# Kernel optimization log

Measured on AMD Instinct MI355X. Metric: run time of the kernel, lower is better.

Reference implementation:

```python
import jax, jax.numpy as jnp
import numpy as np

EMB = 1024

def setup_inputs() -> dict:
    key = jax.random.key(0)
    ks = jax.random.split(key, 6)
    T, k1, k2, D = 64, 256, 1024, EMB
    scale = 1.0 / np.sqrt(D)
    return {
        "fast_feature": jax.random.normal(ks[0], (T, k2, D), jnp.float32),
        "slow_feature": jax.random.normal(ks[1], (T, k1, D), jnp.float32),
        "fast_W": jax.random.normal(ks[2], (D, D), jnp.float32) * scale,
        "fast_b": jax.random.normal(ks[3], (D,), jnp.float32) * 0.01,
        "slow_W": jax.random.normal(ks[4], (D, D), jnp.float32) * scale,
        "slow_b": jax.random.normal(ks[5], (D,), jnp.float32) * 0.01,
    }

def reference(fast_feature, slow_feature, fast_W, fast_b, slow_W, slow_b):
    # Linear projections (torch Linear: x @ W.T + b)
    fast_key = jnp.einsum('tkd,ed->tke', fast_feature, fast_W) + fast_b  # [T,k2,D]
    slow_key = jnp.einsum('tkd,ed->tke', slow_feature, slow_W) + slow_b  # [T,k1,D]
    # Scaled dot-product similarity fast->slow
    sim = jnp.einsum('tqd,tkd->tqk', fast_key, slow_key)  # [T,k2,k1]
    sim = sim / jnp.sqrt(jnp.asarray(slow_feature.shape[-1], sim.dtype))
    attn = jax.nn.softmax(sim, axis=-1)
    ctx = jnp.einsum('tqk,tkd->tqd', attn, slow_feature)  # note: values are raw slow_feature
    return fast_feature + ctx
```

## Files before the change

### kernel.cpp

```cpp
#include <hip/hip_runtime.h>
#include <stdint.h>

typedef __attribute__((ext_vector_type(8))) short bf16x8;
typedef __attribute__((ext_vector_type(4))) float f32x4;

#define BM 128
#define BN 128
#define BK 64

__device__ __forceinline__ unsigned short f2bf(float f) {
  unsigned int u = __builtin_bit_cast(unsigned int, f);
  u += 0x7FFFu + ((u >> 16) & 1u);
  return (unsigned short)(u >> 16);
}

__device__ __forceinline__ void gload_lds16(const void* g, void* l) {
  __builtin_amdgcn_global_load_lds(
      (__attribute__((address_space(1))) void*)(uintptr_t)g,
      (__attribute__((address_space(3))) void*)l,
      16, 0, 0);
}

template <int MODE>
__global__ __launch_bounds__(256, 2) void gemm_bt(
    const unsigned short* __restrict__ A, const unsigned short* __restrict__ B,
    void* __restrict__ Cv, const float* __restrict__ aux, int M, int N, int K,
    int nm, int nn, int nb, long sAB, long sBB, long sCB, long sXB, float scale)
{
  __shared__ __align__(16) unsigned short sAt[BM * BK];
  __shared__ __align__(16) unsigned short sBt[BN * BK];

  const int tid = threadIdx.x;
  const int lane = tid & 63;
  const int wid = tid >> 6;

  int nwg = nm * nn * nb;
  int id = blockIdx.x;
  int swz = (id & 7) * (nwg >> 3) + (id >> 3);
  int t = swz / (nm * nn);
  int rem = swz - t * (nm * nn);
  int mi = rem / nn;
  int ni = rem - mi * nn;

  const long bm = (long)mi * BM;
  const long bn = (long)ni * BN;

  const unsigned short* Ag = A + (long)t * sAB + bm * K;
  const unsigned short* Bg = B + (long)t * sBB + bn * K;

  f32x4 acc[4][4];
#pragma unroll
  for (int i = 0; i < 4; i++)
#pragma unroll
    for (int j = 0; j < 4; j++)
#pragma unroll
      for (int r = 0; r < 4; r++) acc[i][j][r] = 0.f;

  const int wm = (wid >> 1) * 64;
  const int wn = (wid & 1) * 64;
  const int fr = lane & 15;
  const int fq = lane >> 4;

  const int lrow = wid * 32 + (lane >> 3);
  const int lcolb = (lane & 7) * 16;

  for (int k0 = 0; k0 < K; k0 += BK) {
#pragma unroll
    for (int c = 0; c < 4; ++c) {
      int r = lrow + c * 8;
      gload_lds16((const char*)(Ag + (long)r * K + k0) + lcolb,
                  (char*)sAt + wid * 4096 + c * 1024);
      gload_lds16((const char*)(Bg + (long)r * K + k0) + lcolb,
                  (char*)sBt + wid * 4096 + c * 1024);
    }
    __syncthreads();
#pragma unroll
    for (int kk = 0; kk < BK; kk += 32) {
      bf16x8 af[4], bb[4];
#pragma unroll
      for (int i = 0; i < 4; i++)
        af[i] = *(const bf16x8*)&sAt[(wm + i * 16 + fr) * BK + kk + fq * 8];
#pragma unroll
      for (int j = 0; j < 4; j++)
        bb[j] = *(const bf16x8*)&sBt[(wn + j * 16 + fr) * BK + kk + fq * 8];
#pragma unroll
      for (int i = 0; i < 4; i++)
#pragma unroll
        for (int j = 0; j < 4; j++)
          acc[i][j] = __builtin_amdgcn_mfma_f32_16x16x32_bf16(af[i], bb[j], acc[i][j], 0, 0, 0);
    }
    __syncthreads();
  }

#pragma unroll
  for (int i = 0; i < 4; i++) {
    long grow0 = bm + wm + i * 16 + fq * 4;
#pragma unroll
    for (int j = 0; j < 4; j++) {
      long gcol = bn + wn + j * 16 + fr;
      if (MODE == 0) {
        unsigned short* C = (unsigned short*)Cv + (long)t * sCB;
        float b = aux[gcol];
#pragma unroll
        for (int r = 0; r < 4; r++)
          C[(grow0 + r) * N + gcol] = f2bf(acc[i][j][r] + b);
      } else if (MODE == 1) {
        float* C = (float*)Cv + (long)t * sCB;
#pragma unroll
        for (int r = 0; r < 4; r++)
          C[(grow0 + r) * N + gcol] = acc[i][j][r] * scale;
      } else {
        float* C = (float*)Cv + (long)t * sCB;
        const float* X = aux + (long)t * sXB;
#pragma unroll
        for (int r = 0; r < 4; r++) {
          long idx = (grow0 + r) * N + gcol;
          C[idx] = acc[i][j][r] + X[idx];
        }
      }
    }
  }
}

__global__ __launch_bounds__(256) void convert_f32_bf16(
    const float* __restrict__ in, unsigned short* __restrict__ out, long n) {
  long i = ((long)blockIdx.x * 256 + threadIdx.x) * 4;
  long stride = (long)gridDim.x * 1024;
  for (; i < n; i += stride) {
    float4 v = *(const float4*)(in + i);
    ushort4 o;
    o.x = f2bf(v.x); o.y = f2bf(v.y); o.z = f2bf(v.z); o.w = f2bf(v.w);
    *(ushort4*)(out + i) = o;
  }
}

__global__ __launch_bounds__(256) void transpose_slow_bf16(
    const float* __restrict__ in, unsigned short* __restrict__ out) {
  __shared__ unsigned short tile[32][33];
  int t = blockIdx.z;
  int d0 = blockIdx.x * 32;
  int k0 = blockIdx.y * 32;
  const float* ip = in + (long)t * 256 * 1024;
  unsigned short* op = out + (long)t * 1024 * 256;
  int tx = threadIdx.x & 31, ty = threadIdx.x >> 5;
#pragma unroll
  for (int p = 0; p < 4; p++) {
    int k = ty + p * 8;
    tile[k][tx] = f2bf(ip[(long)(k0 + k) * 1024 + d0 + tx]);
  }
  __syncthreads();
#pragma unroll
  for (int p = 0; p < 4; p++) {
    int d = ty + p * 8;
    op[(long)(d0 + d) * 256 + k0 + tx] = tile[tx][d];
  }
}

__global__ __launch_bounds__(256) void softmax256(
    const float* __restrict__ sim, unsigned short* __restrict__ attn) {
  int row = blockIdx.x * 4 + (threadIdx.x >> 6);
  int lane = threadIdx.x & 63;
  const float4 v = *(const float4*)(sim + (long)row * 256 + lane * 4);
  float m = fmaxf(fmaxf(v.x, v.y), fmaxf(v.z, v.w));
#pragma unroll
  for (int o = 32; o >= 1; o >>= 1) m = fmaxf(m, __shfl_xor(m, o));
  float e0 = __expf(v.x - m), e1 = __expf(v.y - m);
  float e2 = __expf(v.z - m), e3 = __expf(v.w - m);
  float s = e0 + e1 + e2 + e3;
#pragma unroll
  for (int o = 32; o >= 1; o >>= 1) s += __shfl_xor(s, o);
  float inv = 1.0f / s;
  ushort4 o4;
  o4.x = f2bf(e0 * inv); o4.y = f2bf(e1 * inv);
  o4.z = f2bf(e2 * inv); o4.w = f2bf(e3 * inv);
  *(ushort4*)(attn + (long)row * 256 + lane * 4) = o4;
}

extern "C" void kernel_launch(void* const* d_in, const int* in_sizes, int n_in,
                              void* d_out, int out_size, void* d_ws, size_t ws_size,
                              hipStream_t stream) {
  const float* fastF     = (const float*)d_in[0];
  const float* slowF     = (const float*)d_in[1];
  const float* fastW     = (const float*)d_in[2];
  const float* fast_bias = (const float*)d_in[3];
  const float* slowW     = (const float*)d_in[4];
  const float* slow_bias = (const float*)d_in[5];
  float* out = (float*)d_out;

  char* ws = (char*)d_ws;
  unsigned short* fastBf  = (unsigned short*)(ws);
  float*          sim     = (float*)(ws);
  unsigned short* attnBf  = (unsigned short*)(ws + 67108864L);
  unsigned short* fastKey = (unsigned short*)(ws + 134217728L);
  unsigned short* slowBf  = (unsigned short*)(ws + 268435456L);
  unsigned short* slowT   = (unsigned short*)(ws + 301989888L);
  unsigned short* slowKey = (unsigned short*)(ws + 335544320L);
  unsigned short* fWb     = (unsigned short*)(ws + 369098752L);
  unsigned short* sWb     = (unsigned short*)(ws + 371195904L);

  convert_f32_bf16<<<2048, 256, 0, stream>>>(fastF, fastBf, 67108864L);
  convert_f32_bf16<<<2048, 256, 0, stream>>>(slowF, slowBf, 16777216L);
  convert_f32_bf16<<<1024, 256, 0, stream>>>(fastW, fWb, 1048576L);
  convert_f32_bf16<<<1024, 256, 0, stream>>>(slowW, sWb, 1048576L);
  transpose_slow_bf16<<<dim3(32, 8, 64), 256, 0, stream>>>(slowF, slowT);

  gemm_bt<0><<<128 * 8, 256, 0, stream>>>(slowBf, sWb, slowKey, slow_bias,
      16384, 1024, 1024, 128, 8, 1, 0, 0, 0, 0, 1.f);
  gemm_bt<0><<<512 * 8, 256, 0, stream>>>(fastBf, fWb, fastKey, fast_bias,
      65536, 1024, 1024, 512, 8, 1, 0, 0, 0, 0, 1.f);
  gemm_bt<1><<<8 * 2 * 64, 256, 0, stream>>>(fastKey, slowKey, sim, nullptr,
      1024, 256, 1024, 8, 2, 64, 1048576L, 262144L, 262144L, 0, 0.03125f);
  softmax256<<<16384, 256, 0, stream>>>(sim, attnBf);
  gemm_bt<2><<<8 * 8 * 64, 256, 0, stream>>>(attnBf, slowT, out, fastF,
      1024, 1024, 256, 8, 8, 64, 262144L, 262144L, 1048576L, 1048576L, 1.f);
}
```

Baseline: 576.6 us.

## Replace GEMM with 256x256 8-wave double-buffered pipelined kernel

Rewrites the batched bf16 GEMM to use 256x256 tiles with 512 threads (8 waves), a 128 KB double-buffered LDS region with XOR-swizzled layout, and staged async global->LDS loads interleaved with MFMA quadrants under explicit vmcnt waits and barriers. Goals are to raise arithmetic intensity per tile, hide global load latency behind compute, and avoid LDS bank conflicts. The cost is larger LDS use, which limits occupancy, and fewer workgroups for the smaller GEMMs (e.g. the sim GEMM has 256 blocks), which may underfill the GPU.

Measured after the change: 497.4 us. 13.7% less time.

```diff
diff --git a/kernel.cpp b/kernel.cpp
--- a/kernel.cpp
+++ b/kernel.cpp
@@ -3,10 +3,6 @@
 
 typedef __attribute__((ext_vector_type(8))) short bf16x8;
 typedef __attribute__((ext_vector_type(4))) float f32x4;
-
-#define BM 128
-#define BN 128
-#define BK 64
 
 __device__ __forceinline__ unsigned short f2bf(float f) {
   unsigned int u = __builtin_bit_cast(unsigned int, f);
@@ -21,105 +17,187 @@
       16, 0, 0);
 }
 
+#define BARRIER() do { asm volatile("" ::: "memory"); __builtin_amdgcn_s_barrier(); asm volatile("" ::: "memory"); } while (0)
+#define WAITVM(N) asm volatile("s_waitcnt vmcnt(" #N ")" ::: "memory")
+
 template <int MODE>
-__global__ __launch_bounds__(256, 2) void gemm_bt(
+__global__ __launch_bounds__(512, 2) void gemm8(
     const unsigned short* __restrict__ A, const unsigned short* __restrict__ B,
-    void* __restrict__ Cv, const float* __restrict__ aux, int M, int N, int K,
-    int nm, int nn, int nb, long sAB, long sBB, long sCB, long sXB, float scale)
+    void* __restrict__ Cv, const float* __restrict__ aux, int N, int K,
+    int nm, int nn, long sAB, long sBB, long sCB, long sXB, float scale)
 {
-  __shared__ __align__(16) unsigned short sAt[BM * BK];
-  __shared__ __align__(16) unsigned short sBt[BN * BK];
+  __shared__ __align__(16) char lds[131072];
+  char* ldsc = lds;
 
   const int tid = threadIdx.x;
   const int lane = tid & 63;
   const int wid = tid >> 6;
-
-  int nwg = nm * nn * nb;
-  int id = blockIdx.x;
-  int swz = (id & 7) * (nwg >> 3) + (id >> 3);
-  int t = swz / (nm * nn);
-  int rem = swz - t * (nm * nn);
-  int mi = rem / nn;
-  int ni = rem - mi * nn;
-
-  const long bm = (long)mi * BM;
-  const long bn = (long)ni * BN;
+  const int fr = lane & 15, fq = lane >> 4;
+
+  const int nwg = gridDim.x;
+  const int id = blockIdx.x;
+  const int swz = (id & 7) * (nwg >> 3) + (id >> 3);
+  const int per = nm * nn;
+  const int t = swz / per;
+  const int rem = swz - t * per;
+  const int mi_ = rem / nn, ni_ = rem - mi_ * nn;
+  const long bm = (long)mi_ * 256, bn = (long)ni_ * 256;
 
   const unsigned short* Ag = A + (long)t * sAB + bm * K;
   const unsigned short* Bg = B + (long)t * sBB + bn * K;
-
-  f32x4 acc[4][4];
-#pragma unroll
-  for (int i = 0; i < 4; i++)
-#pragma unroll
-    for (int j = 0; j < 4; j++)
-#pragma unroll
-      for (int r = 0; r < 4; r++) acc[i][j][r] = 0.f;
-
-  const int wm = (wid >> 1) * 64;
-  const int wn = (wid & 1) * 64;
-  const int fr = lane & 15;
-  const int fq = lane >> 4;
-
-  const int lrow = wid * 32 + (lane >> 3);
-  const int lcolb = (lane & 7) * 16;
-
-  for (int k0 = 0; k0 < K; k0 += BK) {
-#pragma unroll
-    for (int c = 0; c < 4; ++c) {
-      int r = lrow + c * 8;
-      gload_lds16((const char*)(Ag + (long)r * K + k0) + lcolb,
-                  (char*)sAt + wid * 4096 + c * 1024);
-      gload_lds16((const char*)(Bg + (long)r * K + k0) + lcolb,
-                  (char*)sBt + wid * 4096 + c * 1024);
+  const int NT = K >> 6;
+
+  const unsigned short* aS[2][2];
+  const unsigned short* bS[2][2];
+#pragma unroll
+  for (int p = 0; p < 2; ++p) {
+    const int q = p * 512 + tid;
+    const int lr = q >> 3, cs = q & 7;
+    const int cl = cs ^ (lr & 7);
+#pragma unroll
+    for (int h = 0; h < 2; ++h) {
+      const int gA = ((lr >> 6) << 7) | (h << 6) | (lr & 63);
+      const int gB = ((lr >> 5) << 6) | (h << 5) | (lr & 31);
+      aS[p][h] = Ag + (long)gA * K + cl * 8;
+      bS[p][h] = Bg + (long)gB * K + cl * 8;
     }
-    __syncthreads();
-#pragma unroll
-    for (int kk = 0; kk < BK; kk += 32) {
-      bf16x8 af[4], bb[4];
+  }
+
+  const int c0 = ((fq ^ (fr & 3)) + ((fr >> 2) & 1) * 4) * 16;
+  const int aRd = ((wid >> 2) * 64 + fr) * 128 + c0;
+  const int bRd = ((wid & 3) * 32 + fr) * 128 + c0;
+
+  f32x4 acc[2][2][4][2];
+#pragma unroll
+  for (int a = 0; a < 2; a++)
+#pragma unroll
+    for (int b = 0; b < 2; b++)
 #pragma unroll
       for (int i = 0; i < 4; i++)
-        af[i] = *(const bf16x8*)&sAt[(wm + i * 16 + fr) * BK + kk + fq * 8];
-#pragma unroll
-      for (int j = 0; j < 4; j++)
-        bb[j] = *(const bf16x8*)&sBt[(wn + j * 16 + fr) * BK + kk + fq * 8];
-#pragma unroll
-      for (int i = 0; i < 4; i++)
-#pragma unroll
-        for (int j = 0; j < 4; j++)
-          acc[i][j] = __builtin_amdgcn_mfma_f32_16x16x32_bf16(af[i], bb[j], acc[i][j], 0, 0, 0);
+#pragma unroll
+        for (int j = 0; j < 2; j++)
+#pragma unroll
+          for (int r = 0; r < 4; r++) acc[a][b][i][j][r] = 0.f;
+
+  bf16x8 af[4][2], bf[2][2][2];
+
+#define STAGE(srcArr, aoff, h, ktv, b) do {                                   \
+  _Pragma("unroll")                                                           \
+  for (int p = 0; p < 2; ++p)                                                 \
+    gload_lds16(srcArr[p][h] + ((long)(ktv) << 6),                            \
+                ldsc + (aoff) + ((b) << 16) + ((h) << 14) + (p << 13) + (wid << 10)); \
+} while (0)
+
+#define LDA(mi, cub) do {                                                     \
+  _Pragma("unroll")                                                           \
+  for (int i = 0; i < 4; ++i) {                                               \
+    af[i][0] = *(const bf16x8*)(ldsc + (cub) + (mi) * 16384 + aRd + i * 2048);        \
+    af[i][1] = *(const bf16x8*)(ldsc + (cub) + (mi) * 16384 + (aRd ^ 64) + i * 2048); \
+  }                                                                           \
+} while (0)
+
+#define LDB(nj, cub) do {                                                     \
+  _Pragma("unroll")                                                           \
+  for (int j = 0; j < 2; ++j) {                                               \
+    bf[nj][j][0] = *(const bf16x8*)(ldsc + 32768 + (cub) + (nj) * 16384 + bRd + j * 2048);        \
+    bf[nj][j][1] = *(const bf16x8*)(ldsc + 32768 + (cub) + (nj) * 16384 + (bRd ^ 64) + j * 2048); \
+  }                                                                           \
+} while (0)
+
+#define QUAD(mi, nj) do {                                                     \
+  __builtin_amdgcn_s_setprio(1);                                              \
+  _Pragma("unroll")                                                           \
+  for (int i = 0; i < 4; ++i)                                                 \
+  _Pragma("unroll")                                                           \
+  for (int j = 0; j < 2; ++j) {                                               \
+    acc[mi][nj][i][j] = __builtin_amdgcn_mfma_f32_16x16x32_bf16(              \
+        af[i][0], bf[nj][j][0], acc[mi][nj][i][j], 0, 0, 0);                  \
+    acc[mi][nj][i][j] = __builtin_amdgcn_mfma_f32_16x16x32_bf16(              \
+        af[i][1], bf[nj][j][1], acc[mi][nj][i][j], 0, 0, 0);                  \
+  }                                                                           \
+  __builtin_amdgcn_s_setprio(0);                                              \
+} while (0)
+
+  STAGE(aS, 0, 0, 0, 0);
+  STAGE(bS, 32768, 0, 0, 0);
+  STAGE(bS, 32768, 1, 0, 0);
+  STAGE(aS, 0, 1, 0, 0);
+  if (NT > 1) {
+    STAGE(aS, 0, 0, 1, 1);
+    STAGE(bS, 32768, 0, 1, 1);
+    STAGE(bS, 32768, 1, 1, 1);
+    WAITVM(6);
+  } else {
+    WAITVM(0);
+  }
+  BARRIER();
+
+  for (int kt = 0; kt < NT; ++kt) {
+    const int cur = kt & 1, nxt = cur ^ 1;
+    const int cub = cur << 16;
+    LDA(0, cub);
+    LDB(0, cub);
+    if (kt + 1 < NT) STAGE(aS, 0, 1, kt + 1, nxt);
+    BARRIER();
+    QUAD(0, 0);
+    BARRIER();
+    LDB(1, cub);
+    if (kt + 2 < NT) STAGE(aS, 0, 0, kt + 2, cur);
+    BARRIER();
+    QUAD(0, 1);
+    BARRIER();
+    LDA(1, cub);
+    if (kt + 2 < NT) STAGE(bS, 32768, 0, kt + 2, cur);
+    BARRIER();
+    QUAD(1, 0);
+    BARRIER();
+    if (kt + 2 < NT) {
+      STAGE(bS, 32768, 1, kt + 2, cur);
+      QUAD(1, 1);
+      WAITVM(6);
+    } else {
+      QUAD(1, 1);
+      WAITVM(0);
     }
-    __syncthreads();
-  }
-
-#pragma unroll
-  for (int i = 0; i < 4; i++) {
-    long grow0 = bm + wm + i * 16 + fq * 4;
-#pragma unroll
-    for (int j = 0; j < 4; j++) {
-      long gcol = bn + wn + j * 16 + fr;
-      if (MODE == 0) {
-        unsigned short* C = (unsigned short*)Cv + (long)t * sCB;
-        float b = aux[gcol];
-#pragma unroll
-        for (int r = 0; r < 4; r++)
-          C[(grow0 + r) * N + gcol] = f2bf(acc[i][j][r] + b);
-      } else if (MODE == 1) {
-        float* C = (float*)Cv + (long)t * sCB;
-#pragma unroll
-        for (int r = 0; r < 4; r++)
-          C[(grow0 + r) * N + gcol] = acc[i][j][r] * scale;
-      } else {
-        float* C = (float*)Cv + (long)t * sCB;
-        const float* X = aux + (long)t * sXB;
-#pragma unroll
-        for (int r = 0; r < 4; r++) {
-          long idx = (grow0 + r) * N + gcol;
-          C[idx] = acc[i][j][r] + X[idx];
+    BARRIER();
+  }
+
+#pragma unroll
+  for (int mi = 0; mi < 2; ++mi)
+#pragma unroll
+    for (int nj = 0; nj < 2; ++nj)
+#pragma unroll
+      for (int i = 0; i < 4; ++i) {
+        const long grow0 = bm + (wid >> 2) * 128 + mi * 64 + i * 16 + fq * 4;
+#pragma unroll
+        for (int j = 0; j < 2; ++j) {
+          const long gcol = bn + (wid & 3) * 64 + nj * 32 + j * 16 + fr;
+          if (MODE == 0) {
+            unsigned short* C = (unsigned short*)Cv + (long)t * sCB;
+            const float bv = aux[gcol];
+#pragma unroll
+            for (int r = 0; r < 4; ++r)
+              C[(grow0 + r) * N + gcol] = f2bf(acc[mi][nj][i][j][r] + bv);
+          } else if (MODE == 1) {
+            float* C = (float*)Cv + (long)t * sCB;
+#pragma unroll
+            for (int r = 0; r < 4; ++r)
+              C[(grow0 + r) * N + gcol] = acc[mi][nj][i][j][r] * scale;
+          } else {
+            float* C = (float*)Cv + (long)t * sCB;
+            const float* X = aux + (long)t * sXB;
+#pragma unroll
+            for (int r = 0; r < 4; ++r) {
+              const long idx = (grow0 + r) * N + gcol;
+              C[idx] = acc[mi][nj][i][j][r] + X[idx];
+            }
+          }
         }
       }
-    }
-  }
+#undef STAGE
+#undef LDA
+#undef LDB
+#undef QUAD
 }
 
 __global__ __launch_bounds__(256) void convert_f32_bf16(
@@ -204,13 +282,13 @@
   convert_f32_bf16<<<1024, 256, 0, stream>>>(slowW, sWb, 1048576L);
   transpose_slow_bf16<<<dim3(32, 8, 64), 256, 0, stream>>>(slowF, slowT);
 
-  gemm_bt<0><<<128 * 8, 256, 0, stream>>>(slowBf, sWb, slowKey, slow_bias,
-      16384, 1024, 1024, 128, 8, 1, 0, 0, 0, 0, 1.f);
-  gemm_bt<0><<<512 * 8, 256, 0, stream>>>(fastBf, fWb, fastKey, fast_bias,
-      65536, 1024, 1024, 512, 8, 1, 0, 0, 0, 0, 1.f);
-  gemm_bt<1><<<8 * 2 * 64, 256, 0, stream>>>(fastKey, slowKey, sim, nullptr,
-      1024, 256, 1024, 8, 2, 64, 1048576L, 262144L, 262144L, 0, 0.03125f);
+  gemm8<0><<<64 * 4, 512, 0, stream>>>(slowBf, sWb, slowKey, slow_bias,
+      1024, 1024, 64, 4, 0, 0, 0, 0, 1.f);
+  gemm8<0><<<256 * 4, 512, 0, stream>>>(fastBf, fWb, fastKey, fast_bias,
+      1024, 1024, 256, 4, 0, 0, 0, 0, 1.f);
+  gemm8<1><<<4 * 1 * 64, 512, 0, stream>>>(fastKey, slowKey, sim, nullptr,
+      256, 1024, 4, 1, 1048576L, 262144L, 262144L, 0, 0.03125f);
   softmax256<<<16384, 256, 0, stream>>>(sim, attnBf);
-  gemm_bt<2><<<8 * 8 * 64, 256, 0, stream>>>(attnBf, slowT, out, fastF,
-      1024, 1024, 256, 8, 8, 64, 262144L, 262144L, 1048576L, 1048576L, 1.f);
-}
+  gemm8<2><<<4 * 4 * 64, 512, 0, stream>>>(attnBf, slowT, out, fastF,
+      1024, 256, 4, 4, 262144L, 262144L, 1048576L, 1048576L, 1.f);
+}
```
